# Kernel optimization log

Measured on AMD Instinct MI355X. Metric: run time of the kernel, lower is better.

Reference implementation:

```python
import jax, jax.numpy as jnp
import numpy as np

ROUTINGS = 3

def squash(x):
    # x: [..., O]; squash along last dim
    norm = jnp.linalg.norm(x, axis=-1, keepdims=True)
    scale = norm ** 2 / (1 + norm ** 2) / (norm + 1e-9)
    return scale * x

def setup_inputs() -> dict:
    key = jax.random.key(0)
    k1, k2 = jax.random.split(key)
    B, K, I, O, C = 256, 10, 1152, 16, 8
    x = jax.random.normal(k1, (B, I, C), dtype=jnp.float32)
    w = jax.random.normal(k2, (K, I, O, C), dtype=jnp.float32) * 0.05
    return {"x": x, "w": w}

def reference(x, w):
    # x: [B, I, Cin], w: [K, I, O, Cin]
    # u_hat[b,k,i,o] = sum_c w[k,i,o,c] * x[b,i,c]
    u_hat = jnp.einsum('kioc,bic->bkio', w, x)  # [B, K, I, O]
    B, K, I, O = u_hat.shape
    b = jnp.zeros((B, K, I, 1), dtype=u_hat.dtype)
    # routing iterations (fixed small loop); intermediate iters use detached u_hat
    u_hat_d = jax.lax.stop_gradient(u_hat)
    for _ in range(ROUTINGS - 1):
        c = jax.nn.softmax(b, axis=1)              # softmax over output capsules K
        s = jnp.sum(c * u_hat_d, axis=2)           # [B, K, O]
        v = squash(s)                              # [B, K, O]
        uv = jnp.einsum('bkio,bko->bki', u_hat_d, v)[..., None]  # [B, K, I, 1]
        b = b + uv
    c = jax.nn.softmax(b, axis=1)
    s = jnp.sum(c * u_hat, axis=2)
    v = squash(s)
    return v  # [B, K, O]
```

## Files before the change

### kernel.cpp

```cpp
#include <hip/hip_runtime.h>

#define B_ 256
#define K_ 10
#define I_ 1152
#define O_ 16
#define C_ 8
#define BKO (B_*K_*O_)
#define NX 72

static __device__ __forceinline__ unsigned short f32_bf16(float f) {
    unsigned int u = __float_as_uint(f);
    u += 0x7FFFu + ((u >> 16) & 1u);
    return (unsigned short)(u >> 16);
}

template <int CTRL>
static __device__ __forceinline__ float dpp_add(float v) {
    int x = __builtin_amdgcn_update_dpp(0, __float_as_int(v), CTRL, 0xF, 0xF, true);
    return v + __int_as_float(x);
}
static __device__ __forceinline__ float row16_sum(float v) {
    v = dpp_add<0xB1>(v);
    v = dpp_add<0x4E>(v);
    v = dpp_add<0x141>(v);
    v = dpp_add<0x140>(v);
    return v;
}
static __device__ __forceinline__ float quad4_sum(float v) {
    v = dpp_add<0xB1>(v);
    v = dpp_add<0x4E>(v);
    return v;
}

__global__ __launch_bounds__(256) void uhat_kernel(
    const float* __restrict__ x, const float* __restrict__ w,
    unsigned short* __restrict__ u, float* __restrict__ part)
{
    __shared__ float w_lds[16 * 132];
    __shared__ float p_lds[64 * 17];
    const int t   = threadIdx.x;
    const int i_l = t & 15, tg = t >> 4;
    const int i0  = blockIdx.x * 16;
    const int b0  = blockIdx.y * 64 + tg * 4;
    const int k   = blockIdx.z;
    const int i   = i0 + i_l;
    const bool row_leader = (i_l == 0);

    float4 xr[4][2];
#pragma unroll
    for (int bb = 0; bb < 4; bb++) {
        const float4* xp = (const float4*)(x + ((size_t)(b0 + bb) * I_ + i) * C_);
        xr[bb][0] = xp[0];
        xr[bb][1] = xp[1];
    }

    {
        const float4* ws = (const float4*)(w + ((size_t)k * I_ + i0) * O_ * C_);
#pragma unroll
        for (int r = 0; r < 2; r++) {
            int idx = r * 256 + t;
            int ii = idx >> 5, rem = idx & 31;
            *(float4*)&w_lds[ii * 132 + rem * 4] = ws[idx];
        }
    }
    __syncthreads();

    unsigned int pk[4][8];
#pragma unroll
    for (int oo = 0; oo < 8; oo++) {
        float d[4][2];
#pragma unroll
        for (int h = 0; h < 2; h++) {
            const int o = oo * 2 + h;
            const float4 w0 = *(const float4*)&w_lds[i_l * 132 + o * 8];
            const float4 w1 = *(const float4*)&w_lds[i_l * 132 + o * 8 + 4];
#pragma unroll
            for (int bb = 0; bb < 4; bb++) {
                d[bb][h] = w0.x*xr[bb][0].x + w0.y*xr[bb][0].y
                         + w0.z*xr[bb][0].z + w0.w*xr[bb][0].w
                         + w1.x*xr[bb][1].x + w1.y*xr[bb][1].y
                         + w1.z*xr[bb][1].z + w1.w*xr[bb][1].w;
            }
        }
#pragma unroll
        for (int bb = 0; bb < 4; bb++) {
#pragma unroll
            for (int h = 0; h < 2; h++) {
                const float rs = row16_sum(d[bb][h]);
                if (row_leader)
                    p_lds[(tg * 4 + bb) * 17 + oo * 2 + h] = rs;
            }
        }
#pragma unroll
        for (int bb = 0; bb < 4; bb++)
            pk[bb][oo] = (unsigned int)f32_bf16(d[bb][0]) |
                         ((unsigned int)f32_bf16(d[bb][1]) << 16);
    }
#pragma unroll
    for (int bb = 0; bb < 4; bb++) {
        unsigned int* dst = (unsigned int*)
            (u + (((size_t)(b0 + bb) * K_ + k) * I_ + i) * O_);
        *(uint4*)(dst)     = make_uint4(pk[bb][0], pk[bb][1], pk[bb][2], pk[bb][3]);
        *(uint4*)(dst + 4) = make_uint4(pk[bb][4], pk[bb][5], pk[bb][6], pk[bb][7]);
    }

    __syncthreads();
    {
        const int bl = t >> 2, o4 = (t & 3) * 4;
        float4 v;
        v.x = p_lds[bl * 17 + o4 + 0];
        v.y = p_lds[bl * 17 + o4 + 1];
        v.z = p_lds[bl * 17 + o4 + 2];
        v.w = p_lds[bl * 17 + o4 + 3];
        *(float4*)&part[(((size_t)blockIdx.x * K_ + k) * 256
                         + blockIdx.y * 64 + bl) * O_ + o4] = v;
    }
}

static __device__ __forceinline__ void sweep(
    const unsigned short* __restrict__ ub, int i_l,
    const float* __restrict__ v_lds, int og, float acc[K_][4])
{
#pragma unroll
    for (int k = 0; k < K_; k++)
#pragma unroll
        for (int j = 0; j < 4; j++) acc[k][j] = 0.f;

    uint2 P[K_], Q[K_];
#pragma unroll
    for (int k = 0; k < K_; k++)
        P[k] = *(const uint2*)(ub + ((size_t)k * I_ + i_l) * O_);

#pragma unroll 1
    for (int ic = 0; ic < 9; ic++) {
        if (ic + 1 < 9) {
            const int i = (ic + 1) * 128 + i_l;
#pragma unroll
            for (int k = 0; k < K_; k++)
                Q[k] = *(const uint2*)(ub + ((size_t)k * I_ + i) * O_);
        }
        float c[K_];
        float Z = 0.f;
#pragma unroll
        for (int k = 0; k < K_; k++) {
            const float f0 = __uint_as_float(P[k].x << 16);
            const float f1 = __uint_as_float(P[k].x & 0xffff0000u);
            const float f2 = __uint_as_float(P[k].y << 16);
            const float f3 = __uint_as_float(P[k].y & 0xffff0000u);
            const float* vk = &v_lds[k * 16 + og * 4];
            float lk = f0 * vk[0] + f1 * vk[1] + f2 * vk[2] + f3 * vk[3];
            lk = quad4_sum(lk);
            c[k] = __expf(lk);
            Z += c[k];
        }
        const float inv = 1.0f / Z;
#pragma unroll
        for (int k = 0; k < K_; k++) {
            const float ck = c[k] * inv;
            acc[k][0] = fmaf(ck, __uint_as_float(P[k].x << 16),        acc[k][0]);
            acc[k][1] = fmaf(ck, __uint_as_float(P[k].x & 0xffff0000u), acc[k][1]);
            acc[k][2] = fmaf(ck, __uint_as_float(P[k].y << 16),        acc[k][2]);
            acc[k][3] = fmaf(ck, __uint_as_float(P[k].y & 0xffff0000u), acc[k][3]);
        }
#pragma unroll
        for (int k = 0; k < K_; k++) P[k] = Q[k];
    }
}

static __device__ __forceinline__ void block_reduce(
    float acc[K_][4], float* __restrict__ red, int lane, int wv)
{
#pragma unroll
    for (int k = 0; k < K_; k++)
#pragma unroll
        for (int j = 0; j < 4; j++) {
            float a = acc[k][j];
            a += __shfl_xor(a, 4);  a += __shfl_xor(a, 8);
            a += __shfl_xor(a, 16); a += __shfl_xor(a, 32);
            acc[k][j] = a;
        }
    if (lane < 4) {
#pragma unroll
        for (int k = 0; k < K_; k++)
            *(float4*)&red[wv * 160 + k * 16 + lane * 4] =
                make_float4(acc[k][0], acc[k][1], acc[k][2], acc[k][3]);
    }
    __syncthreads();
}

static __device__ __forceinline__ float sum8(const float* __restrict__ red, int t)
{
    float s = 0.f;
#pragma unroll
    for (int wgi = 0; wgi < 8; wgi++) s += red[wgi * 160 + t];
    return s;
}

static __device__ __forceinline__ float squash_v(float s) {
    float n2 = s * s;
    n2 += __shfl_xor(n2, 1); n2 += __shfl_xor(n2, 2);
    n2 += __shfl_xor(n2, 4); n2 += __shfl_xor(n2, 8);
    const float norm = sqrtf(n2);
    return s * (n2 / (1.0f + n2) / (norm + 1e-9f));
}

__global__ __launch_bounds__(512) void route_all(
    const unsigned short* __restrict__ u, const float* __restrict__ part,
    float* __restrict__ out)
{
    __shared__ float red[8 * 160];
    __shared__ float v_lds[160];
    __shared__ float v1_lds[160];

    const int t    = threadIdx.x;
    const int og   = t & 3, i_l = t >> 2;
    const int b    = blockIdx.x;
    const int lane = t & 63, wv = t >> 6;

    const unsigned short* ub = u + (size_t)b * K_ * I_ * O_ + og * 4;
    float acc[K_][4];

    if (t < 160) {
        const int k = t >> 4, o = t & 15;
        const float* pb = part + ((size_t)k * 256 + b) * O_ + o;
        float s = 0.f;
#pragma unroll
        for (int xb = 0; xb < NX; xb++)
            s += pb[(size_t)xb * BKO];
        float v = squash_v(s * (1.0f / K_));
        v1_lds[t] = v;
        v_lds[t]  = v;
    }
    __syncthreads();

    sweep(ub, i_l, v_lds, og, acc);
    block_reduce(acc, red, lane, wv);
    float v12 = 0.f;
    if (t < 160) v12 = v1_lds[t] + squash_v(sum8(red, t));
    __syncthreads();
    if (t < 160) v_lds[t] = v12;
    __syncthreads();

    sweep(ub, i_l, v_lds, og, acc);
    block_reduce(acc, red, lane, wv);
    if (t < 160)
        out[(size_t)b * 160 + t] = squash_v(sum8(red, t));
}

extern "C" void kernel_launch(void* const* d_in, const int* in_sizes, int n_in,
                              void* d_out, int out_size, void* d_ws, size_t ws_size,
                              hipStream_t stream)
{
    const float* x = (const float*)d_in[0];
    const float* w = (const float*)d_in[1];
    float* outp = (float*)d_out;

    float* part = (float*)d_ws;
    unsigned short* u = (unsigned short*)(part + (size_t)NX * BKO);

    uhat_kernel<<<dim3(72, 4, 10), 256, 0, stream>>>(x, w, u, part);
    route_all<<<B_, 512, 0, stream>>>(u, part, outp);
}
```

Measured before the change: 123.6 us.

## Double-buffer u_hat chunks into LDS via global_load_lds in routing sweep

The routing sweep now stages each 128-row chunk of bf16 u_hat for all K into a pair of 40 KB LDS buffers using direct global-to-LDS loads, prefetching the next chunk while computing on the current one. It replaces the per-thread register prefetch, and the v vector is hoisted into registers once per sweep. The aim is to hide global-load latency with asynchronous DMA-style loads and cut register pressure. In exchange it uses about 80 KB of LDS per block, which limits occupancy, and adds a block-wide barrier per chunk. It also relies on correct ordering of the async LDS writes before the barrier.

```diff
diff --git a/kernel.cpp b/kernel.cpp
--- a/kernel.cpp
+++ b/kernel.cpp
@@ -117,53 +117,74 @@
     }
 }
 
-static __device__ __forceinline__ void sweep(
-    const unsigned short* __restrict__ ub, int i_l,
-    const float* __restrict__ v_lds, int og, float acc[K_][4])
-{
+
+static __device__ __forceinline__ void stage_chunk(
+    const unsigned short* __restrict__ ub0,
+    int chunk, int t, char* lds_buf)
+{
+    const int i0 = chunk * 128;
+#pragma unroll
+    for (int r = 0; r < 5; r++) {
+        const int L   = r * 512 + t;
+        const int k   = L >> 8;
+        const int rem = L & 255;
+        const unsigned short* src = ub0 + ((size_t)k * I_ + i0) * O_ + rem * 8;
+        char* dst = lds_buf + ((size_t)(r * 512 + (t & ~63)) * 16);
+        __builtin_amdgcn_global_load_lds(
+            (const __attribute__((address_space(1))) unsigned int*)src,
+            (__attribute__((address_space(3))) unsigned int*)dst,
+            16, 0, 0);
+    }
+}
+
+static __device__ __forceinline__ void sweep_lds(
+    const unsigned short* __restrict__ ub0, int t, int i_l, int og,
+    const float* __restrict__ v_lds, float acc[K_][4],
+    char* __restrict__ ubuf0, char* __restrict__ ubuf1)
+{
+    float4 vr[K_];
 #pragma unroll
     for (int k = 0; k < K_; k++)
+        vr[k] = *(const float4*)&v_lds[k * 16 + og * 4];
+
+#pragma unroll
+    for (int k = 0; k < K_; k++)
 #pragma unroll
         for (int j = 0; j < 4; j++) acc[k][j] = 0.f;
 
-    uint2 P[K_], Q[K_];
-#pragma unroll
-    for (int k = 0; k < K_; k++)
-        P[k] = *(const uint2*)(ub + ((size_t)k * I_ + i_l) * O_);
-
+    stage_chunk(ub0, 0, t, ubuf0);
+    __syncthreads();
+
+    const int boff = i_l * 32 + og * 8;
 #pragma unroll 1
-    for (int ic = 0; ic < 9; ic++) {
-        if (ic + 1 < 9) {
-            const int i = (ic + 1) * 128 + i_l;
-#pragma unroll
-            for (int k = 0; k < K_; k++)
-                Q[k] = *(const uint2*)(ub + ((size_t)k * I_ + i) * O_);
-        }
-        float c[K_];
-        float Z = 0.f;
+    for (int j = 0; j < 9; j++) {
+        char* cur = (j & 1) ? ubuf1 : ubuf0;
+        char* nxt = (j & 1) ? ubuf0 : ubuf1;
+        if (j < 8) stage_chunk(ub0, j + 1, t, nxt);
+
+        float c_[K_]; float Z = 0.f;
 #pragma unroll
         for (int k = 0; k < K_; k++) {
-            const float f0 = __uint_as_float(P[k].x << 16);
-            const float f1 = __uint_as_float(P[k].x & 0xffff0000u);
-            const float f2 = __uint_as_float(P[k].y << 16);
-            const float f3 = __uint_as_float(P[k].y & 0xffff0000u);
-            const float* vk = &v_lds[k * 16 + og * 4];
-            float lk = f0 * vk[0] + f1 * vk[1] + f2 * vk[2] + f3 * vk[3];
+            const uint2 P = *(const uint2*)(cur + k * 4096 + boff);
+            const float f0 = __uint_as_float(P.x << 16);
+            const float f1 = __uint_as_float(P.x & 0xffff0000u);
+            const float f2 = __uint_as_float(P.y << 16);
+            const float f3 = __uint_as_float(P.y & 0xffff0000u);
+            float lk = f0*vr[k].x + f1*vr[k].y + f2*vr[k].z + f3*vr[k].w;
             lk = quad4_sum(lk);
-            c[k] = __expf(lk);
-            Z += c[k];
+            c_[k] = __expf(lk); Z += c_[k];
         }
         const float inv = 1.0f / Z;
 #pragma unroll
         for (int k = 0; k < K_; k++) {
-            const float ck = c[k] * inv;
-            acc[k][0] = fmaf(ck, __uint_as_float(P[k].x << 16),        acc[k][0]);
-            acc[k][1] = fmaf(ck, __uint_as_float(P[k].x & 0xffff0000u), acc[k][1]);
-            acc[k][2] = fmaf(ck, __uint_as_float(P[k].y << 16),        acc[k][2]);
-            acc[k][3] = fmaf(ck, __uint_as_float(P[k].y & 0xffff0000u), acc[k][3]);
-        }
-#pragma unroll
-        for (int k = 0; k < K_; k++) P[k] = Q[k];
+            const uint2 P = *(const uint2*)(cur + k * 4096 + boff);
+            const float ck = c_[k] * inv;
+            acc[k][0] = fmaf(ck, __uint_as_float(P.x << 16),         acc[k][0]);
+            acc[k][1] = fmaf(ck, __uint_as_float(P.x & 0xffff0000u), acc[k][1]);
+            acc[k][2] = fmaf(ck, __uint_as_float(P.y << 16),         acc[k][2]);
+            acc[k][3] = fmaf(ck, __uint_as_float(P.y & 0xffff0000u), acc[k][3]);
+        }
+        __syncthreads();
     }
 }
 
@@ -208,6 +229,7 @@
     const unsigned short* __restrict__ u, const float* __restrict__ part,
     float* __restrict__ out)
 {
+    __shared__ __align__(16) char ubuf[2][40960];
     __shared__ float red[8 * 160];
     __shared__ float v_lds[160];
     __shared__ float v1_lds[160];
@@ -217,7 +239,7 @@
     const int b    = blockIdx.x;
     const int lane = t & 63, wv = t >> 6;
 
-    const unsigned short* ub = u + (size_t)b * K_ * I_ * O_ + og * 4;
+    const unsigned short* ub0 = u + (size_t)b * K_ * I_ * O_;
     float acc[K_][4];
 
     if (t < 160) {
@@ -233,7 +255,7 @@
     }
     __syncthreads();
 
-    sweep(ub, i_l, v_lds, og, acc);
+    sweep_lds(ub0, t, i_l, og, v_lds, acc, ubuf[0], ubuf[1]);
     block_reduce(acc, red, lane, wv);
     float v12 = 0.f;
     if (t < 160) v12 = v1_lds[t] + squash_v(sum8(red, t));
@@ -241,7 +263,7 @@
     if (t < 160) v_lds[t] = v12;
     __syncthreads();
 
-    sweep(ub, i_l, v_lds, og, acc);
+    sweep_lds(ub0, t, i_l, og, v_lds, acc, ubuf[0], ubuf[1]);
     block_reduce(acc, red, lane, wv);
     if (t < 160)
         out[(size_t)b * 160 + t] = squash_v(sum8(red, t));
```

New measurement: 125.5 us. No clear change (+1.5%).
